# Kernel tuning notes

Hardware: AMD Instinct MI355X
Metric: run time of the kernel (lower is better)

## Reference

```python
import jax, jax.numpy as jnp
import numpy as np

B, N, EN, C, F, HEADS, DE = 2, 8192, 16, 256, 512, 8, 8
D = C // HEADS  # att_size = 32
TAU = 0.1


def _xavier(k, shape):
    lim = float(np.sqrt(6.0 / (shape[0] + shape[1])))
    return jax.random.uniform(k, shape, jnp.float32, -lim, lim)


def setup_inputs() -> dict:
    key = jax.random.key(0)
    ks = jax.random.split(key, 16)
    return {
        "xyz": jax.random.normal(ks[0], (B, N, 3), jnp.float32),
        "features": jax.random.normal(ks[1], (B, C, N), jnp.float32),
        "edges": jax.random.randint(ks[2], (B, N * EN, 2), 0, N),
        "gumbel_u": jax.random.uniform(ks[3], (B * N, DE, EN), jnp.float32, 1e-6, 1.0 - 1e-6),
        "g1": jnp.ones((C,), jnp.float32), "be1": jnp.zeros((C,), jnp.float32),
        "Wq": _xavier(ks[4], (C, C)),
        "Wk": _xavier(ks[5], (C + 3, C)),
        "Wv": _xavier(ks[6], (C + 3, C)),
        "Wo": _xavier(ks[7], (C, C)),
        "g2": jnp.ones((C,), jnp.float32), "be2": jnp.zeros((C,), jnp.float32),
        "W1": _xavier(ks[8], (C, F)), "bf1": jnp.zeros((F,), jnp.float32),
        "W2": _xavier(ks[9], (F, C)), "bf2": jnp.zeros((C,), jnp.float32),
        "D1": _xavier(ks[10], (C, C // 2)), "db1": jnp.zeros((C // 2,), jnp.float32),
        "D2": _xavier(ks[11], (C // 2, DE)), "db2": jnp.zeros((DE,), jnp.float32),
    }


def _ln(x, g, b):
    m = jnp.mean(x, -1, keepdims=True)
    v = jnp.mean((x - m) ** 2, -1, keepdims=True)
    return (x - m) * jax.lax.rsqrt(v + 1e-6) * g + b


def reference(xyz, features, edges, gumbel_u, g1, be1, Wq, Wk, Wv, Wo,
              g2, be2, W1, bf1, W2, bf2, D1, db1, D2, db2):
    feats = jnp.transpose(features, (0, 2, 1))            # b,n,C
    x = _ln(feats, g1, be1)
    idx = edges[:, :, 0]                                  # b, n*EN (neighbor ids)
    gather = jax.vmap(lambda a, i: a[i])
    sf = gather(x, idx).reshape(B, N, EN, C)              # neighbor features
    sc = gather(xyz, idx).reshape(B, N, EN, 3)            # neighbor coords
    # learned gumbel-softmax downsample: EN -> DE edges per node
    sf2 = sf.reshape(B * N, EN, C)
    h = jax.nn.relu(sf2 @ D1 + db1) @ D2 + db2            # (B*N, EN, DE)
    logits = jnp.transpose(h, (0, 2, 1))                  # (B*N, DE, EN)
    gnoise = -jnp.log(-jnp.log(gumbel_u))
    w = jax.nn.softmax((logits + gnoise) / TAU, axis=-1)
    sf = jnp.einsum('bde,bec->bdc', w, sf2).reshape(B, N, DE, C)
    sc = jnp.einsum('bde,bec->bdc', w, sc.reshape(B * N, EN, 3)).reshape(B, N, DE, 3)
    s = jnp.concatenate([sf, sc - xyz[:, :, None, :]], axis=-1)  # b,n,DE,C+3
    # local neighbor multi-head attention
    k = (s @ Wk).reshape(B, N, DE, HEADS, D)
    v = (s @ Wv).reshape(B, N, DE, HEADS, D)
    q = (x @ Wq).reshape(B, N, HEADS, D)
    simi = jnp.einsum('bnehd,bnhd->bneh', k, q) * (1.0 / float(np.sqrt(D)))
    sm = jax.nn.softmax(simi, axis=2)                     # over neighbor axis
    o = jnp.einsum('bnehd,bneh->bnhd', v, sm).reshape(B, N, C) @ Wo
    feats = feats + o
    y = _ln(feats, g2, be2)
    y = jax.nn.relu(y @ W1 + bf1) @ W2 + bf2
    feats = feats + y
    return jnp.transpose(feats, (0, 2, 1))
```

## Files before the change

### kernel.cpp

```cpp
#include <hip/hip_runtime.h>
#include <math.h>

#define NB 8192
#define CC 256

using bf16x8 = __attribute__((ext_vector_type(8))) short;
using f32x4  = __attribute__((ext_vector_type(4))) float;

__device__ inline ushort f2b(float f) {
  union { float f; unsigned u; } v; v.f = f;
  unsigned u = v.u;
  u += 0x7FFF + ((u >> 16) & 1);
  return (ushort)(u >> 16);
}

__global__ __launch_bounds__(256) void wpackT(const float* __restrict__ Wk, const float* __restrict__ Wv,
                                              const float* __restrict__ Wq, const float* __restrict__ Wo,
                                              const float* __restrict__ W1, const float* __restrict__ W2,
                                              ushort* __restrict__ WtKVQ, ushort* __restrict__ WtO,
                                              ushort* __restrict__ Wt1, ushort* __restrict__ Wt2) {
  int i = blockIdx.x * 256 + threadIdx.x;
  if (i < 196608) {
    int n = i >> 8, k = i & 255;
    float v = (n < 256) ? Wk[(size_t)k * 256 + n]
            : (n < 512) ? Wv[(size_t)k * 256 + (n - 256)]
                        : Wq[(size_t)k * 256 + (n - 512)];
    WtKVQ[(size_t)n * 256 + k] = f2b(v);
  } else if (i < 262144) {
    int j = i - 196608; int n = j >> 8, k = j & 255;
    WtO[(size_t)n * 256 + k] = f2b(Wo[(size_t)k * 256 + n]);
  } else if (i < 393216) {
    int j = i - 262144; int n = j >> 8, k = j & 255;
    Wt1[(size_t)n * 256 + k] = f2b(W1[(size_t)k * 512 + n]);
  } else {
    int j = i - 393216; int n = j >> 9, k = j & 511;
    Wt2[(size_t)n * 512 + k] = f2b(W2[(size_t)k * 256 + n]);
  }
}

__global__ __launch_bounds__(256) void k1_ln1(const float* __restrict__ features,
                                              const float* __restrict__ g1,
                                              const float* __restrict__ be1,
                                              float* __restrict__ X,
                                              float* __restrict__ F) {
  __shared__ float tile[256][36];
  int b = blockIdx.y;
  int n0 = blockIdx.x * 32;
  int t = threadIdx.x;
  int tn = t & 31, ch = t >> 5;
  for (int cb = 0; cb < 32; ++cb) {
    int c = cb * 8 + ch;
    tile[c][tn] = features[((size_t)b * 256 + c) * NB + n0 + tn];
  }
  __syncthreads();
  int tok = t >> 3, sub = t & 7;
  float s = 0.f, ss = 0.f;
  #pragma unroll
  for (int k = 0; k < 32; ++k) {
    float v = tile[sub + 8 * k][tok];
    s += v; ss += v * v;
  }
  #pragma unroll
  for (int m = 1; m < 8; m <<= 1) { s += __shfl_xor(s, m); ss += __shfl_xor(ss, m); }
  float mean = s * (1.f / 256.f);
  float var  = ss * (1.f / 256.f) - mean * mean;
  float rstd = rsqrtf(var + 1e-6f);
  size_t row = ((size_t)b * NB + n0 + tok) * 256;
  for (int k = 0; k < 32; ++k) {
    int c = sub + 8 * k;
    float v = tile[c][tok];
    F[row + c] = v;
    X[row + c] = (v - mean) * rstd * g1[c] + be1[c];
  }
}

__global__ __launch_bounds__(256) void gemm128(
    const float* __restrict__ A, int lda,
    const float* __restrict__ Bm, int ldb,
    float* __restrict__ Cc, int ldc,
    int K,
    const float* __restrict__ bias, int relu,
    const float* __restrict__ resid, int ldr,
    const float* __restrict__ mrs, const float* __restrict__ lg, const float* __restrict__ lb)
{
  __shared__ __align__(16) float As[16][132];
  __shared__ __align__(16) float Bs[16][132];
  int m0 = blockIdx.y * 128, n0 = blockIdx.x * 128;
  int t = threadIdx.x;
  int ty = t >> 4, tx = t & 15;
  float acc[2][2][4][4] = {};
  int ar  = t >> 2, ak4 = (t & 3) * 4;
  int bk  = t >> 5, bn4 = (t & 31) * 4;
  for (int k0 = 0; k0 < K; k0 += 16) {
    #pragma unroll
    for (int p = 0; p < 2; ++p) {
      int r = ar + 64 * p;
      float4 av = *(const float4*)&A[(size_t)(m0 + r) * lda + k0 + ak4];
      if (mrs) {
        float mean = mrs[(m0 + r) * 2], rstd = mrs[(m0 + r) * 2 + 1];
        av.x = (av.x - mean) * rstd * lg[k0 + ak4 + 0] + lb[k0 + ak4 + 0];
        av.y = (av.y - mean) * rstd * lg[k0 + ak4 + 1] + lb[k0 + ak4 + 1];
        av.z = (av.z - mean) * rstd * lg[k0 + ak4 + 2] + lb[k0 + ak4 + 2];
        av.w = (av.w - mean) * rstd * lg[k0 + ak4 + 3] + lb[k0 + ak4 + 3];
      }
      As[ak4 + 0][r] = av.x; As[ak4 + 1][r] = av.y;
      As[ak4 + 2][r] = av.z; As[ak4 + 3][r] = av.w;
    }
    #pragma unroll
    for (int p = 0; p < 2; ++p) {
      int kk = bk + 8 * p;
      *(float4*)&Bs[kk][bn4] = *(const float4*)&Bm[(size_t)(k0 + kk) * ldb + n0 + bn4];
    }
    __syncthreads();
    #pragma unroll
    for (int kk = 0; kk < 16; ++kk) {
      float4 a0 = *(const float4*)&As[kk][ty * 4];
      float4 a1 = *(const float4*)&As[kk][64 + ty * 4];
      float4 b0 = *(const float4*)&Bs[kk][tx * 4];
      float4 b1 = *(const float4*)&Bs[kk][64 + tx * 4];
      float am[2][4] = {{a0.x, a0.y, a0.z, a0.w}, {a1.x, a1.y, a1.z, a1.w}};
      float bv[2][4] = {{b0.x, b0.y, b0.z, b0.w}, {b1.x, b1.y, b1.z, b1.w}};
      #pragma unroll
      for (int h = 0; h < 2; ++h)
        #pragma unroll
        for (int g = 0; g < 2; ++g)
          #pragma unroll
          for (int i = 0; i < 4; ++i)
            #pragma unroll
            for (int j = 0; j < 4; ++j)
              acc[h][g][i][j] += am[h][i] * bv[g][j];
    }
    __syncthreads();
  }
  #pragma unroll
  for (int h = 0; h < 2; ++h)
    #pragma unroll
    for (int i = 0; i < 4; ++i) {
      size_t m = m0 + 64 * h + ty * 4 + i;
      #pragma unroll
      for (int g = 0; g < 2; ++g) {
        int nb = n0 + 64 * g + tx * 4;
        float vals[4];
        #pragma unroll
        for (int j = 0; j < 4; ++j) {
          float v = acc[h][g][i][j];
          if (bias) v += bias[nb + j];
          if (relu) v = fmaxf(v, 0.f);
          vals[j] = v;
        }
        if (resid) {
          float4 rv = *(const float4*)&resid[m * (size_t)ldr + nb];
          vals[0] += rv.x; vals[1] += rv.y; vals[2] += rv.z; vals[3] += rv.w;
        }
        float4 o4; o4.x = vals[0]; o4.y = vals[1]; o4.z = vals[2]; o4.w = vals[3];
        *(float4*)&Cc[m * (size_t)ldc + nb] = o4;
      }
    }
}

__global__ __launch_bounds__(256) void gemm_mfma(
    const float* __restrict__ A, int lda,
    const ushort* __restrict__ Bt,
    float* __restrict__ Cc, int ldc,
    int K,
    const float* __restrict__ bias, int relu,
    const float* __restrict__ resid, int ldr,
    const float* __restrict__ mrs, const float* __restrict__ lg, const float* __restrict__ lb)
{
  __shared__ __align__(16) ushort As[128 * 32];
  __shared__ __align__(16) ushort Bs[128 * 32];
  int t = threadIdx.x;
  int m0 = blockIdx.y * 128, n0 = blockIdx.x * 128;
  int wv = t >> 6, lane = t & 63;
  int wm = wv >> 1, wn = wv & 1;
  int lr = lane & 15, kg = lane >> 4;
  f32x4 acc[4][4];
  #pragma unroll
  for (int i = 0; i < 4; ++i)
    #pragma unroll
    for (int j = 0; j < 4; ++j)
      acc[i][j] = (f32x4)0.0f;

  for (int k0 = 0; k0 < K; k0 += 32) {
    #pragma unroll
    for (int p = 0; p < 2; ++p) {
      int c = t + p * 256;
      int m = c >> 2, kq = c & 3;
      const float* src = &A[(size_t)(m0 + m) * lda + k0 + kq * 8];
      float v[8];
      *(float4*)&v[0] = *(const float4*)src;
      *(float4*)&v[4] = *(const float4*)(src + 4);
      if (mrs) {
        float mean = mrs[(m0 + m) * 2], rstd = mrs[(m0 + m) * 2 + 1];
        #pragma unroll
        for (int j = 0; j < 8; ++j) {
          int kk = k0 + kq * 8 + j;
          v[j] = (v[j] - mean) * rstd * lg[kk] + lb[kk];
        }
      }
      ushort o[8];
      #pragma unroll
      for (int j = 0; j < 8; ++j) o[j] = f2b(v[j]);
      *(uint4*)&As[m * 32 + (kq ^ ((m >> 1) & 3)) * 8] = *(uint4*)o;
    }
    #pragma unroll
    for (int p = 0; p < 2; ++p) {
      int c = t + p * 256;
      int n = c >> 2, kq = c & 3;
      uint4 w = *(const uint4*)&Bt[(size_t)(n0 + n) * K + k0 + kq * 8];
      *(uint4*)&Bs[n * 32 + (kq ^ ((n >> 1) & 3)) * 8] = w;
    }
    __syncthreads();
    bf16x8 af[4], bfr[4];
    #pragma unroll
    for (int mi = 0; mi < 4; ++mi) {
      int m = wm * 64 + mi * 16 + lr;
      af[mi] = *(const bf16x8*)&As[m * 32 + (kg ^ ((m >> 1) & 3)) * 8];
    }
    #pragma unroll
    for (int ni = 0; ni < 4; ++ni) {
      int n = wn * 64 + ni * 16 + lr;
      bfr[ni] = *(const bf16x8*)&Bs[n * 32 + (kg ^ ((n >> 1) & 3)) * 8];
    }
    #pragma unroll
    for (int mi = 0; mi < 4; ++mi)
      #pragma unroll
      for (int ni = 0; ni < 4; ++ni)
        acc[mi][ni] = __builtin_amdgcn_mfma_f32_16x16x32_bf16(af[mi], bfr[ni], acc[mi][ni], 0, 0, 0);
    __syncthreads();
  }
  #pragma unroll
  for (int ni = 0; ni < 4; ++ni) {
    int col = n0 + wn * 64 + ni * 16 + lr;
    float bv = bias ? bias[col] : 0.f;
    #pragma unroll
    for (int mi = 0; mi < 4; ++mi) {
      #pragma unroll
      for (int r = 0; r < 4; ++r) {
        int row = m0 + wm * 64 + mi * 16 + kg * 4 + r;
        float v = acc[mi][ni][r] + bv;
        if (relu) v = fmaxf(v, 0.f);
        if (resid) v += resid[(size_t)row * ldr + col];
        Cc[(size_t)row * ldc + col] = v;
      }
    }
  }
}

__global__ __launch_bounds__(256) void k3_wave(
    const float* __restrict__ XC,
    const int* __restrict__ edges,
    const float* __restrict__ gu,
    const float* __restrict__ xyz,
    const float* __restrict__ Wk, const float* __restrict__ Wv,
    const float* __restrict__ D2, const float* __restrict__ db2,
    float* __restrict__ O)
{
  __shared__ float d2s[1024];
  int t = threadIdx.x;
  for (int i = t; i < 1024; i += 256) {
    int f = i >> 3, d = i & 7;
    d2s[f * 8 + (d ^ (f >> 5))] = D2[i];
  }
  __syncthreads();

  int wv = t >> 6, lane = t & 63;
  int b = blockIdx.y;
  int n = blockIdx.x * 4 + wv;
  size_t bn = (size_t)b * NB + n;
  int e = lane >> 2, fq = lane & 3;

  int idx = edges[(bn * 16 + e) * 2];
  size_t rowE = ((size_t)b * NB + idx) * 896;

  float acc[8] = {0.f, 0.f, 0.f, 0.f, 0.f, 0.f, 0.f, 0.f};
  const float4* xd4 = (const float4*)(XC + rowE + fq * 32);
  #pragma unroll
  for (int i = 0; i < 8; ++i) {
    float4 xd = xd4[i];
    float xv[4] = {fmaxf(xd.x, 0.f), fmaxf(xd.y, 0.f), fmaxf(xd.z, 0.f), fmaxf(xd.w, 0.f)};
    #pragma unroll
    for (int j = 0; j < 4; ++j) {
      int f = fq * 32 + i * 4 + j;
      #pragma unroll
      for (int d = 0; d < 8; ++d)
        acc[d] += xv[j] * d2s[f * 8 + (d ^ fq)];
    }
  }
  #pragma unroll
  for (int d = 0; d < 8; ++d) {
    acc[d] += __shfl_xor(acc[d], 1);
    acc[d] += __shfl_xor(acc[d], 2);
    acc[d] += db2[d];
  }

  float w[8];
  #pragma unroll
  for (int d = 0; d < 8; ++d) {
    float u = gu[(bn * 8 + d) * 16 + e];
    float gn = -logf(-logf(u));
    float val = (acc[d] + gn) * 10.0f;
    float mx = val;
    mx = fmaxf(mx, __shfl_xor(mx, 4));
    mx = fmaxf(mx, __shfl_xor(mx, 8));
    mx = fmaxf(mx, __shfl_xor(mx, 16));
    mx = fmaxf(mx, __shfl_xor(mx, 32));
    float ex = expf(val - mx);
    float sm = ex;
    sm += __shfl_xor(sm, 4);
    sm += __shfl_xor(sm, 8);
    sm += __shfl_xor(sm, 16);
    sm += __shfl_xor(sm, 32);
    w[d] = ex / sm;
  }

  float xg = (fq < 3) ? xyz[((size_t)b * NB + idx) * 3 + fq] : 0.f;
  float xo = (fq < 3) ? xyz[bn * 3 + fq] : 0.f;
  float scw[8];
  #pragma unroll
  for (int d = 0; d < 8; ++d) {
    float s = w[d] * xg;
    s += __shfl_xor(s, 4);
    s += __shfl_xor(s, 8);
    s += __shfl_xor(s, 16);
    s += __shfl_xor(s, 32);
    scw[d] = s - xo;
  }

  float4 kk[8], vv[8];
  #pragma unroll
  for (int d = 0; d < 8; ++d) {
    kk[d].x = kk[d].y = kk[d].z = kk[d].w = 0.f;
    vv[d].x = vv[d].y = vv[d].z = vv[d].w = 0.f;
  }
  #pragma unroll
  for (int j = 0; j < 3; ++j) {
    float4 wkb = *(const float4*)&Wk[(size_t)(256 + j) * 256 + lane * 4];
    float4 wvb = *(const float4*)&Wv[(size_t)(256 + j) * 256 + lane * 4];
    #pragma unroll
    for (int d = 0; d < 8; ++d) {
      float sc = __shfl(scw[d], (lane & ~3) | j);
      kk[d].x += sc * wkb.x; kk[d].y += sc * wkb.y; kk[d].z += sc * wkb.z; kk[d].w += sc * wkb.w;
      vv[d].x += sc * wvb.x; vv[d].y += sc * wvb.y; vv[d].z += sc * wvb.z; vv[d].w += sc * wvb.w;
    }
  }
  #pragma unroll 4
  for (int ee = 0; ee < 16; ++ee) {
    int eidx = __shfl(idx, ee * 4);
    size_t rE = ((size_t)b * NB + eidx) * 896;
    float4 xk = ((const float4*)(XC + rE + 128))[lane];
    float4 xv = ((const float4*)(XC + rE + 384))[lane];
    #pragma unroll
    for (int d = 0; d < 8; ++d) {
      float wd = __shfl(w[d], ee * 4);
      kk[d].x += wd * xk.x; kk[d].y += wd * xk.y; kk[d].z += wd * xk.z; kk[d].w += wd * xk.w;
      vv[d].x += wd * xv.x; vv[d].y += wd * xv.y; vv[d].z += wd * xv.z; vv[d].w += wd * xv.w;
    }
  }

  float4 q = ((const float4*)(XC + bn * 896 + 640))[lane];
  float sim[8];
  #pragma unroll
  for (int d = 0; d < 8; ++d) {
    float p = q.x * kk[d].x + q.y * kk[d].y + q.z * kk[d].z + q.w * kk[d].w;
    p += __shfl_xor(p, 1);
    p += __shfl_xor(p, 2);
    p += __shfl_xor(p, 4);
    sim[d] = p * 0.17677669529663687f;
  }
  float mx = sim[0];
  #pragma unroll
  for (int d = 1; d < 8; ++d) mx = fmaxf(mx, sim[d]);
  float e8[8], sume = 0.f;
  #pragma unroll
  for (int d = 0; d < 8; ++d) { e8[d] = expf(sim[d] - mx); sume += e8[d]; }
  float inv = 1.f / sume;
  float4 oc; oc.x = oc.y = oc.z = oc.w = 0.f;
  #pragma unroll
  for (int d = 0; d < 8; ++d) {
    float sm = e8[d] * inv;
    oc.x += vv[d].x * sm; oc.y += vv[d].y * sm; oc.z += vv[d].z * sm; oc.w += vv[d].w * sm;
  }
  ((float4*)(O + bn * 256))[lane] = oc;
}

__global__ __launch_bounds__(256) void k5a_stats(const float* __restrict__ F, float* __restrict__ MRS) {
  int wave = threadIdx.x >> 6, lane = threadIdx.x & 63;
  size_t row = (size_t)blockIdx.x * 4 + wave;
  float4 v4 = *(const float4*)&F[row * 256 + lane * 4];
  float s = v4.x + v4.y + v4.z + v4.w;
  float ss = v4.x * v4.x + v4.y * v4.y + v4.z * v4.z + v4.w * v4.w;
  #pragma unroll
  for (int m = 1; m < 64; m <<= 1) { s += __shfl_xor(s, m); ss += __shfl_xor(ss, m); }
  if (lane == 0) {
    float mean = s * (1.f / 256.f);
    float var = ss * (1.f / 256.f) - mean * mean;
    MRS[row * 2] = mean;
    MRS[row * 2 + 1] = rsqrtf(var + 1e-6f);
  }
}

__global__ __launch_bounds__(256) void k7_transpose(const float* __restrict__ F, float* __restrict__ out) {
  __shared__ float tile[32][33];
  int b = blockIdx.z;
  int c0 = blockIdx.y * 32;
  int n0 = blockIdx.x * 32;
  int t = threadIdx.x;
  int nl = t >> 5, cl = t & 31;
  #pragma unroll
  for (int i = 0; i < 4; ++i) {
    int nn = nl + i * 8;
    tile[nn][cl] = F[((size_t)b * NB + n0 + nn) * 256 + c0 + cl];
  }
  __syncthreads();
  int cl2 = t >> 5, nl2 = t & 31;
  #pragma unroll
  for (int i = 0; i < 4; ++i) {
    int cc = cl2 + i * 8;
    out[((size_t)b * 256 + c0 + cc) * NB + n0 + nl2] = tile[nl2][cc];
  }
}

extern "C" void kernel_launch(void* const* d_in, const int* in_sizes, int n_in,
                              void* d_out, int out_size, void* d_ws, size_t ws_size,
                              hipStream_t stream) {
  const float* xyz      = (const float*)d_in[0];
  const float* features = (const float*)d_in[1];
  const int*   edges    = (const int*)d_in[2];
  const float* gu       = (const float*)d_in[3];
  const float* g1       = (const float*)d_in[4];
  const float* be1      = (const float*)d_in[5];
  const float* Wq       = (const float*)d_in[6];
  const float* Wk       = (const float*)d_in[7];
  const float* Wv       = (const float*)d_in[8];
  const float* Wo       = (const float*)d_in[9];
  const float* g2       = (const float*)d_in[10];
  const float* be2      = (const float*)d_in[11];
  const float* W1       = (const float*)d_in[12];
  const float* bf1      = (const float*)d_in[13];
  const float* W2       = (const float*)d_in[14];
  const float* bf2      = (const float*)d_in[15];
  const float* D1       = (const float*)d_in[16];
  const float* db1      = (const float*)d_in[17];
  const float* D2       = (const float*)d_in[18];
  const float* db2      = (const float*)d_in[19];
  float* out = (float*)d_out;
  float* ws  = (float*)d_ws;

  float* X    = ws;
  float* F    = ws + 4194304;
  float* XC   = ws + 8388608;
  float* O    = X;
  float* Y1   = XC;
  ushort* WtKVQ = (ushort*)out;
  ushort* WtO   = WtKVQ + 196608;
  ushort* Wt1   = WtO + 65536;
  ushort* Wt2   = Wt1 + 131072;
  float*  MRS   = out + 262144;

  wpackT<<<2048, 256, 0, stream>>>(Wk, Wv, Wq, Wo, W1, W2, WtKVQ, WtO, Wt1, Wt2);

  k1_ln1<<<dim3(256, 2), 256, 0, stream>>>(features, g1, be1, X, F);

  gemm128<<<dim3(1, 128), 256, 0, stream>>>(X, 256, D1, 128, XC, 896, 256, db1, 0, nullptr, 0, nullptr, nullptr, nullptr);

  gemm_mfma<<<dim3(6, 128), 256, 0, stream>>>(X, 256, WtKVQ, XC + 128, 896, 256, nullptr, 0, nullptr, 0, nullptr, nullptr, nullptr);

  k3_wave<<<dim3(2048, 2), 256, 0, stream>>>(XC, edges, gu, xyz, Wk, Wv, D2, db2, O);

  gemm_mfma<<<dim3(2, 128), 256, 0, stream>>>(O, 256, WtO, F, 256, 256, nullptr, 0, F, 256, nullptr, nullptr, nullptr);

  k5a_stats<<<4096, 256, 0, stream>>>(F, MRS);

  gemm_mfma<<<dim3(4, 128), 256, 0, stream>>>(F, 256, Wt1, Y1, 512, 256, bf1, 1, nullptr, 0, MRS, g2, be2);

  gemm_mfma<<<dim3(2, 128), 256, 0, stream>>>(Y1, 512, Wt2, F, 256, 512, bf2, 0, F, 256, nullptr, nullptr, nullptr);

  k7_transpose<<<dim3(256, 8, 2), 256, 0, stream>>>(F, out);
}
```

Baseline: 379.3 us.

## Use split-bf16 MFMA for D1 GEMM and store K/V projections as bf16

Replaces the scalar fp32 D1 GEMM with an MFMA kernel that emulates fp32 accuracy through hi/lo bf16 splits and three MFMAs per tile. The K/V projection now writes bf16 output into a separate compact buffer, and Q gets its own fp32 buffer, so the gather-heavy attention kernel reads half the bytes per neighbour row. This lowers gather bandwidth and GEMM compute in exchange for reduced precision of the gathered K/V values.

```diff
diff --git a/kernel.cpp b/kernel.cpp
--- a/kernel.cpp
+++ b/kernel.cpp
@@ -13,12 +13,20 @@
   u += 0x7FFF + ((u >> 16) & 1);
   return (ushort)(u >> 16);
 }
+__device__ inline float b2f(ushort h) {
+  union { unsigned u; float f; } v; v.u = ((unsigned)h) << 16; return v.f;
+}
+__device__ inline float u2f(unsigned u) {
+  union { unsigned u; float f; } v; v.u = u; return v.f;
+}
 
 __global__ __launch_bounds__(256) void wpackT(const float* __restrict__ Wk, const float* __restrict__ Wv,
                                               const float* __restrict__ Wq, const float* __restrict__ Wo,
                                               const float* __restrict__ W1, const float* __restrict__ W2,
+                                              const float* __restrict__ D1,
                                               ushort* __restrict__ WtKVQ, ushort* __restrict__ WtO,
-                                              ushort* __restrict__ Wt1, ushort* __restrict__ Wt2) {
+                                              ushort* __restrict__ Wt1, ushort* __restrict__ Wt2,
+                                              ushort* __restrict__ D1hi, ushort* __restrict__ D1lo) {
   int i = blockIdx.x * 256 + threadIdx.x;
   if (i < 196608) {
     int n = i >> 8, k = i & 255;
@@ -32,9 +40,17 @@
   } else if (i < 393216) {
     int j = i - 262144; int n = j >> 8, k = j & 255;
     Wt1[(size_t)n * 256 + k] = f2b(W1[(size_t)k * 512 + n]);
-  } else {
+  } else if (i < 524288) {
     int j = i - 393216; int n = j >> 9, k = j & 511;
     Wt2[(size_t)n * 512 + k] = f2b(W2[(size_t)k * 256 + n]);
+  } else if (i < 557056) {
+    int j = i - 524288; int n = j >> 8, k = j & 255;
+    D1hi[(size_t)n * 256 + k] = f2b(D1[(size_t)k * 128 + n]);
+  } else {
+    int j = i - 557056; int n = j >> 8, k = j & 255;
+    float v = D1[(size_t)k * 128 + n];
+    ushort hi = f2b(v);
+    D1lo[(size_t)n * 256 + k] = f2b(v - b2f(hi));
   }
 }
 
@@ -74,88 +90,89 @@
   }
 }
 
-__global__ __launch_bounds__(256) void gemm128(
+__global__ __launch_bounds__(256) void gemm_mfma_x2(
     const float* __restrict__ A, int lda,
-    const float* __restrict__ Bm, int ldb,
-    float* __restrict__ Cc, int ldc,
-    int K,
-    const float* __restrict__ bias, int relu,
-    const float* __restrict__ resid, int ldr,
-    const float* __restrict__ mrs, const float* __restrict__ lg, const float* __restrict__ lb)
+    const ushort* __restrict__ Bhi, const ushort* __restrict__ Blo,
+    float* __restrict__ Cc, int ldc, int K,
+    const float* __restrict__ bias)
 {
-  __shared__ __align__(16) float As[16][132];
-  __shared__ __align__(16) float Bs[16][132];
-  int m0 = blockIdx.y * 128, n0 = blockIdx.x * 128;
+  __shared__ __align__(16) ushort Ah[128 * 32], Al[128 * 32], Bh[128 * 32], Bl[128 * 32];
   int t = threadIdx.x;
-  int ty = t >> 4, tx = t & 15;
-  float acc[2][2][4][4] = {};
-  int ar  = t >> 2, ak4 = (t & 3) * 4;
-  int bk  = t >> 5, bn4 = (t & 31) * 4;
-  for (int k0 = 0; k0 < K; k0 += 16) {
+  int m0 = blockIdx.y * 128;
+  int wv = t >> 6, lane = t & 63;
+  int wm = wv >> 1, wn = wv & 1;
+  int lr = lane & 15, kg = lane >> 4;
+  f32x4 acc[4][4];
+  #pragma unroll
+  for (int i = 0; i < 4; ++i)
+    #pragma unroll
+    for (int j = 0; j < 4; ++j) acc[i][j] = (f32x4)0.0f;
+
+  for (int k0 = 0; k0 < K; k0 += 32) {
     #pragma unroll
     for (int p = 0; p < 2; ++p) {
-      int r = ar + 64 * p;
-      float4 av = *(const float4*)&A[(size_t)(m0 + r) * lda + k0 + ak4];
-      if (mrs) {
-        float mean = mrs[(m0 + r) * 2], rstd = mrs[(m0 + r) * 2 + 1];
-        av.x = (av.x - mean) * rstd * lg[k0 + ak4 + 0] + lb[k0 + ak4 + 0];
-        av.y = (av.y - mean) * rstd * lg[k0 + ak4 + 1] + lb[k0 + ak4 + 1];
-        av.z = (av.z - mean) * rstd * lg[k0 + ak4 + 2] + lb[k0 + ak4 + 2];
-        av.w = (av.w - mean) * rstd * lg[k0 + ak4 + 3] + lb[k0 + ak4 + 3];
+      int c = t + p * 256;
+      int m = c >> 2, kq = c & 3;
+      const float* src = &A[(size_t)(m0 + m) * lda + k0 + kq * 8];
+      float v[8];
+      *(float4*)&v[0] = *(const float4*)src;
+      *(float4*)&v[4] = *(const float4*)(src + 4);
+      ushort hi[8], lo[8];
+      #pragma unroll
+      for (int j = 0; j < 8; ++j) {
+        hi[j] = f2b(v[j]);
+        lo[j] = f2b(v[j] - b2f(hi[j]));
       }
-      As[ak4 + 0][r] = av.x; As[ak4 + 1][r] = av.y;
-      As[ak4 + 2][r] = av.z; As[ak4 + 3][r] = av.w;
+      int off = m * 32 + (kq ^ ((m >> 1) & 3)) * 8;
+      *(uint4*)&Ah[off] = *(uint4*)hi;
+      *(uint4*)&Al[off] = *(uint4*)lo;
     }
     #pragma unroll
     for (int p = 0; p < 2; ++p) {
-      int kk = bk + 8 * p;
-      *(float4*)&Bs[kk][bn4] = *(const float4*)&Bm[(size_t)(k0 + kk) * ldb + n0 + bn4];
+      int c = t + p * 256;
+      int n = c >> 2, kq = c & 3;
+      int off = n * 32 + (kq ^ ((n >> 1) & 3)) * 8;
+      *(uint4*)&Bh[off] = *(const uint4*)&Bhi[(size_t)n * K + k0 + kq * 8];
+      *(uint4*)&Bl[off] = *(const uint4*)&Blo[(size_t)n * K + k0 + kq * 8];
     }
     __syncthreads();
-    #pragma unroll
-    for (int kk = 0; kk < 16; ++kk) {
-      float4 a0 = *(const float4*)&As[kk][ty * 4];
-      float4 a1 = *(const float4*)&As[kk][64 + ty * 4];
-      float4 b0 = *(const float4*)&Bs[kk][tx * 4];
-      float4 b1 = *(const float4*)&Bs[kk][64 + tx * 4];
-      float am[2][4] = {{a0.x, a0.y, a0.z, a0.w}, {a1.x, a1.y, a1.z, a1.w}};
-      float bv[2][4] = {{b0.x, b0.y, b0.z, b0.w}, {b1.x, b1.y, b1.z, b1.w}};
-      #pragma unroll
-      for (int h = 0; h < 2; ++h)
-        #pragma unroll
-        for (int g = 0; g < 2; ++g)
-          #pragma unroll
-          for (int i = 0; i < 4; ++i)
-            #pragma unroll
-            for (int j = 0; j < 4; ++j)
-              acc[h][g][i][j] += am[h][i] * bv[g][j];
-    }
+    bf16x8 ahi[4], alo[4], bhi[4], blo[4];
+    #pragma unroll
+    for (int mi = 0; mi < 4; ++mi) {
+      int m = wm * 64 + mi * 16 + lr;
+      int off = m * 32 + (kg ^ ((m >> 1) & 3)) * 8;
+      ahi[mi] = *(const bf16x8*)&Ah[off];
+      alo[mi] = *(const bf16x8*)&Al[off];
+    }
+    #pragma unroll
+    for (int ni = 0; ni < 4; ++ni) {
+      int n = wn * 64 + ni * 16 + lr;
+      int off = n * 32 + (kg ^ ((n >> 1) & 3)) * 8;
+      bhi[ni] = *(const bf16x8*)&Bh[off];
+      blo[ni] = *(const bf16x8*)&Bl[off];
+    }
+    #pragma unroll
+    for (int mi = 0; mi < 4; ++mi)
+      #pragma unroll
+      for (int ni = 0; ni < 4; ++ni) {
+        acc[mi][ni] = __builtin_amdgcn_mfma_f32_16x16x32_bf16(ahi[mi], bhi[ni], acc[mi][ni], 0, 0, 0);
+        acc[mi][ni] = __builtin_amdgcn_mfma_f32_16x16x32_bf16(ahi[mi], blo[ni], acc[mi][ni], 0, 0, 0);
+        acc[mi][ni] = __builtin_amdgcn_mfma_f32_16x16x32_bf16(alo[mi], bhi[ni], acc[mi][ni], 0, 0, 0);
+      }
     __syncthreads();
   }
   #pragma unroll
-  for (int h = 0; h < 2; ++h)
-    #pragma unroll
-    for (int i = 0; i < 4; ++i) {
-      size_t m = m0 + 64 * h + ty * 4 + i;
-      #pragma unroll
-      for (int g = 0; g < 2; ++g) {
-        int nb = n0 + 64 * g + tx * 4;
-        float vals[4];
-        #pragma unroll
-        for (int j = 0; j < 4; ++j) {
-          float v = acc[h][g][i][j];
-          if (bias) v += bias[nb + j];
-          if (relu) v = fmaxf(v, 0.f);
-          vals[j] = v;
-        }
-        if (resid) {
-          float4 rv = *(const float4*)&resid[m * (size_t)ldr + nb];
-          vals[0] += rv.x; vals[1] += rv.y; vals[2] += rv.z; vals[3] += rv.w;
-        }
-        float4 o4; o4.x = vals[0]; o4.y = vals[1]; o4.z = vals[2]; o4.w = vals[3];
-        *(float4*)&Cc[m * (size_t)ldc + nb] = o4;
+  for (int ni = 0; ni < 4; ++ni) {
+    int col = wn * 64 + ni * 16 + lr;
+    float bv = bias[col];
+    #pragma unroll
+    for (int mi = 0; mi < 4; ++mi)
+      #pragma unroll
+      for (int r = 0; r < 4; ++r) {
+        int row = m0 + wm * 64 + mi * 16 + kg * 4 + r;
+        Cc[(size_t)row * ldc + col] = acc[mi][ni][r] + bv;
       }
-    }
+  }
 }
 
 __global__ __launch_bounds__(256) void gemm_mfma(
@@ -178,8 +195,7 @@
   #pragma unroll
   for (int i = 0; i < 4; ++i)
     #pragma unroll
-    for (int j = 0; j < 4; ++j)
-      acc[i][j] = (f32x4)0.0f;
+    for (int j = 0; j < 4; ++j) acc[i][j] = (f32x4)0.0f;
 
   for (int k0 = 0; k0 < K; k0 += 32) {
     #pragma unroll
@@ -247,8 +263,81 @@
   }
 }
 
+__global__ __launch_bounds__(256) void gemm_mfma_b16o(
+    const float* __restrict__ A, int lda,
+    const ushort* __restrict__ Bt,
+    ushort* __restrict__ Cc, int ldc, int K)
+{
+  __shared__ __align__(16) ushort As[128 * 32];
+  __shared__ __align__(16) ushort Bs[128 * 32];
+  int t = threadIdx.x;
+  int m0 = blockIdx.y * 128, n0 = blockIdx.x * 128;
+  int wv = t >> 6, lane = t & 63;
+  int wm = wv >> 1, wn = wv & 1;
+  int lr = lane & 15, kg = lane >> 4;
+  f32x4 acc[4][4];
+  #pragma unroll
+  for (int i = 0; i < 4; ++i)
+    #pragma unroll
+    for (int j = 0; j < 4; ++j) acc[i][j] = (f32x4)0.0f;
+
+  for (int k0 = 0; k0 < K; k0 += 32) {
+    #pragma unroll
+    for (int p = 0; p < 2; ++p) {
+      int c = t + p * 256;
+      int m = c >> 2, kq = c & 3;
+      const float* src = &A[(size_t)(m0 + m) * lda + k0 + kq * 8];
+      float v[8];
+      *(float4*)&v[0] = *(const float4*)src;
+      *(float4*)&v[4] = *(const float4*)(src + 4);
+      ushort o[8];
+      #pragma unroll
+      for (int j = 0; j < 8; ++j) o[j] = f2b(v[j]);
+      *(uint4*)&As[m * 32 + (kq ^ ((m >> 1) & 3)) * 8] = *(uint4*)o;
+    }
+    #pragma unroll
+    for (int p = 0; p < 2; ++p) {
+      int c = t + p * 256;
+      int n = c >> 2, kq = c & 3;
+      uint4 w = *(const uint4*)&Bt[(size_t)(n0 + n) * K + k0 + kq * 8];
+      *(uint4*)&Bs[n * 32 + (kq ^ ((n >> 1) & 3)) * 8] = w;
+    }
+    __syncthreads();
+    bf16x8 af[4], bfr[4];
+    #pragma unroll
+    for (int mi = 0; mi < 4; ++mi) {
+      int m = wm * 64 + mi * 16 + lr;
+      af[mi] = *(const bf16x8*)&As[m * 32 + (kg ^ ((m >> 1) & 3)) * 8];
+    }
+    #pragma unroll
+    for (int ni = 0; ni < 4; ++ni) {
+      int n = wn * 64 + ni * 16 + lr;
+      bfr[ni] = *(const bf16x8*)&Bs[n * 32 + (kg ^ ((n >> 1) & 3)) * 8];
+    }
+    #pragma unroll
+    for (int mi = 0; mi < 4; ++mi)
+      #pragma unroll
+      for (int ni = 0; ni < 4; ++ni)
+        acc[mi][ni] = __builtin_amdgcn_mfma_f32_16x16x32_bf16(af[mi], bfr[ni], acc[mi][ni], 0, 0, 0);
+    __syncthreads();
+  }
+  #pragma unroll
+  for (int ni = 0; ni < 4; ++ni) {
+    int col = n0 + wn * 64 + ni * 16 + lr;
+    #pragma unroll
+    for (int mi = 0; mi < 4; ++mi)
+      #pragma unroll
+      for (int r = 0; r < 4; ++r) {
+        int row = m0 + wm * 64 + mi * 16 + kg * 4 + r;
+        Cc[(size_t)row * ldc + col] = f2b(acc[mi][ni][r]);
+      }
+  }
+}
+
 __global__ __launch_bounds__(256) void k3_wave(
-    const float* __restrict__ XC,
+    const float* __restrict__ XD,
+    const ushort* __restrict__ XKV,
+    const float* __restrict__ XQ,
     const int* __restrict__ edges,
     const float* __restrict__ gu,
     const float* __restrict__ xyz,
@@ -271,10 +360,9 @@
   int e = lane >> 2, fq = lane & 3;
 
   int idx = edges[(bn * 16 + e) * 2];
-  size_t rowE = ((size_t)b * NB + idx) * 896;
 
   float acc[8] = {0.f, 0.f, 0.f, 0.f, 0.f, 0.f, 0.f, 0.f};
-  const float4* xd4 = (const float4*)(XC + rowE + fq * 32);
+  const float4* xd4 = (const float4*)(XD + ((size_t)b * NB + idx) * 128 + fq * 32);
   #pragma unroll
   for (int i = 0; i < 8; ++i) {
     float4 xd = xd4[i];
@@ -344,21 +432,25 @@
       vv[d].x += sc * wvb.x; vv[d].y += sc * wvb.y; vv[d].z += sc * wvb.z; vv[d].w += sc * wvb.w;
     }
   }
-  #pragma unroll 4
+  #pragma unroll 8
   for (int ee = 0; ee < 16; ++ee) {
     int eidx = __shfl(idx, ee * 4);
-    size_t rE = ((size_t)b * NB + eidx) * 896;
-    float4 xk = ((const float4*)(XC + rE + 128))[lane];
-    float4 xv = ((const float4*)(XC + rE + 384))[lane];
+    const ushort* rE = XKV + ((size_t)b * NB + eidx) * 512;
+    uint2 ku = *(const uint2*)(rE + lane * 4);
+    uint2 vu = *(const uint2*)(rE + 256 + lane * 4);
+    float xk0 = u2f(ku.x << 16), xk1 = u2f(ku.x & 0xFFFF0000u);
+    float xk2 = u2f(ku.y << 16), xk3 = u2f(ku.y & 0xFFFF0000u);
+    float xv0 = u2f(vu.x << 16), xv1 = u2f(vu.x & 0xFFFF0000u);
+    float xv2 = u2f(vu.y << 16), xv3 = u2f(vu.y & 0xFFFF0000u);
     #pragma unroll
     for (int d = 0; d < 8; ++d) {
       float wd = __shfl(w[d], ee * 4);
-      kk[d].x += wd * xk.x; kk[d].y += wd * xk.y; kk[d].z += wd * xk.z; kk[d].w += wd * xk.w;
-      vv[d].x += wd * xv.x; vv[d].y += wd * xv.y; vv[d].z += wd * xv.z; vv[d].w += wd * xv.w;
-    }
-  }
-
-  float4 q = ((const float4*)(XC + bn * 896 + 640))[lane];
+      kk[d].x += wd * xk0; kk[d].y += wd * xk1; kk[d].z += wd * xk2; kk[d].w += wd * xk3;
+      vv[d].x += wd * xv0; vv[d].y += wd * xv1; vv[d].z += wd * xv2; vv[d].w += wd * xv3;
+    }
+  }
+
+  float4 q = ((const float4*)(XQ + bn * 256))[lane];
   float sim[8];
   #pragma unroll
   for (int d = 0; d < 8; ++d) {
@@ -447,34 +539,45 @@
   float* out = (float*)d_out;
   float* ws  = (float*)d_ws;
 
-  float* X    = ws;
-  float* F    = ws + 4194304;
-  float* XC   = ws + 8388608;
-  float* O    = X;
-  float* Y1   = XC;
+  float*  X   = ws;
+  float*  F   = ws + 4194304;
+  float*  XD  = ws + 8388608;
+  ushort* XKV = (ushort*)(ws + 10485760);
+  float*  XQ  = ws + 14680064;
+  float*  O   = X;
+  float*  Y1  = ws + 8388608;
+
   ushort* WtKVQ = (ushort*)out;
   ushort* WtO   = WtKVQ + 196608;
   ushort* Wt1   = WtO + 65536;
   ushort* Wt2   = Wt1 + 131072;
-  float*  MRS   = out + 262144;
-
-  wpackT<<<2048, 256, 0, stream>>>(Wk, Wv, Wq, Wo, W1, W2, WtKVQ, WtO, Wt1, Wt2);
+  ushort* D1hi  = Wt2 + 131072;
+  ushort* D1lo  = D1hi + 32768;
+  float*  MRS   = out + 294912;
+
+  wpackT<<<2304, 256, 0, stream>>>(Wk, Wv, Wq, Wo, W1, W2, D1, WtKVQ, WtO, Wt1, Wt2, D1hi, D1lo);
 
   k1_ln1<<<dim3(256, 2), 256, 0, stream>>>(features, g1, be1, X, F);
 
-  gemm128<<<dim3(1, 128), 256, 0, stream>>>(X, 256, D1, 128, XC, 896, 256, db1, 0, nullptr, 0, nullptr, nullptr, nullptr);
-
-  gemm_mfma<<<dim3(6, 128), 256, 0, stream>>>(X, 256, WtKVQ, XC + 128, 896, 256, nullptr, 0, nullptr, 0, nullptr, nullptr, nullptr);
-
-  k3_wave<<<dim3(2048, 2), 256, 0, stream>>>(XC, edges, gu, xyz, Wk, Wv, D2, db2, O);
-
-  gemm_mfma<<<dim3(2, 128), 256, 0, stream>>>(O, 256, WtO, F, 256, 256, nullptr, 0, F, 256, nullptr, nullptr, nullptr);
+  gemm_mfma_x2<<<dim3(1, 128), 256, 0, stream>>>(X, 256, D1hi, D1lo, XD, 128, 256, db1);
+
+  gemm_mfma_b16o<<<dim3(4, 128), 256, 0, stream>>>(X, 256, WtKVQ, XKV, 512, 256);
+
+  gemm_mfma<<<dim3(2, 128), 256, 0, stream>>>(X, 256, WtKVQ + 512 * 256, XQ, 256, 256,
+                                              nullptr, 0, nullptr, 0, nullptr, nullptr, nullptr);
+
+  k3_wave<<<dim3(2048, 2), 256, 0, stream>>>(XD, XKV, XQ, edges, gu, xyz, Wk, Wv, D2, db2, O);
+
+  gemm_mfma<<<dim3(2, 128), 256, 0, stream>>>(O, 256, WtO, F, 256, 256,
+                                              nullptr, 0, F, 256, nullptr, nullptr, nullptr);
 
   k5a_stats<<<4096, 256, 0, stream>>>(F, MRS);
 
-  gemm_mfma<<<dim3(4, 128), 256, 0, stream>>>(F, 256, Wt1, Y1, 512, 256, bf1, 1, nullptr, 0, MRS, g2, be2);
-
-  gemm_mfma<<<dim3(2, 128), 256, 0, stream>>>(Y1, 512, Wt2, F, 256, 512, bf2, 0, F, 256, nullptr, nullptr, nullptr);
+  gemm_mfma<<<dim3(4, 128), 256, 0, stream>>>(F, 256, Wt1, Y1, 512, 256,
+                                              bf1, 1, nullptr, 0, MRS, g2, be2);
+
+  gemm_mfma<<<dim3(2, 128), 256, 0, stream>>>(Y1, 512, Wt2, F, 256, 512,
+                                              bf2, 0, F, 256, nullptr, nullptr, nullptr);
 
   k7_transpose<<<dim3(256, 8, 2), 256, 0, stream>>>(F, out);
 }
```

Result: faster. 356.0 us (-6.2%).
